# Kernel optimization log

Measured on AMD Instinct MI355X. Metric: run time of the kernel, lower is better.

## Reference

```python
import jax, jax.numpy as jnp
import numpy as np

NUM_NODES = 4
D = 1024            # hidden dim and dims of s_0, s_1; initial_input_dims = [D, D, 2D]
NUM_OPS = 5         # candidate ops per MixedLayer: linear, relu, tanh, sigmoid, leaky_relu(0.2)
NUM_LAYERS = 18     # sum_{i<4} (i+3)
BATCH = 4096

_ACTS = [
    lambda h: h,
    jax.nn.relu,
    jnp.tanh,
    jax.nn.sigmoid,
    lambda h: jax.nn.leaky_relu(h, 0.2),
]

def setup_inputs() -> dict:
    key = jax.random.key(0)
    ks = jax.random.split(key, 7)
    s_0 = jax.random.normal(ks[0], (BATCH, D), jnp.float32)
    s_1 = jax.random.normal(ks[1], (BATCH, D), jnp.float32)
    genotype = jax.random.uniform(ks[2], (NUM_LAYERS, NUM_OPS), jnp.float32)
    genotype = genotype / genotype.sum(-1, keepdims=True)  # softmax-like arch weights
    scale = 1.0 / np.sqrt(D)
    # 14 layers take a D-dim input; 4 layers (the cat(s_0,s_1) edge of each node) take 2D
    Ws = jax.random.normal(ks[3], (14, NUM_OPS, D, D), jnp.float32) * scale
    Wb = jax.random.normal(ks[4], (4, NUM_OPS, 2 * D, D), jnp.float32) * (scale / np.sqrt(2.0))
    bs = jax.random.normal(ks[5], (NUM_LAYERS, NUM_OPS, D), jnp.float32) * 0.01
    return {"s_0": s_0, "s_1": s_1, "genotype": genotype, "Ws": Ws, "Wb": Wb, "bs": bs}

def _mixed(x, W, b, w):
    # x: [B, in], W: [K, in, D], b: [K, D], w: [K]
    h = jnp.einsum('bi,kio->kbo', x, W) + b[:, None, :]
    out = 0.0
    for k, act in enumerate(_ACTS):
        out = out + w[k] * act(h[k])
    return out

def reference(s_0, s_1, genotype, Ws, Wb, bs):
    states = [s_0, s_1, jnp.concatenate([s_0, s_1], axis=-1)]
    offset, si, bi = 0, 0, 0
    for i in range(NUM_NODES):
        s = 0.0
        for j, cur in enumerate(states):
            l = offset + j
            if j == 2:  # edge from cat(s_0, s_1): input dim 2D
                W = Wb[bi]; bi += 1
            else:
                W = Ws[si]; si += 1
            s = s + _mixed(cur, W, bs[l], genotype[l])
        offset += len(states)
        states.append(s)
    return states[-1]
```

## Files before the change

### kernel.cpp

```cpp
#include <hip/hip_runtime.h>
#include <hip/hip_bf16.h>
#include <cstdint>
#include <cstddef>

typedef __attribute__((ext_vector_type(8))) short bf16x8;
typedef __attribute__((ext_vector_type(4))) float f32x4;

#define DEV __device__ __forceinline__

DEV unsigned short f2bf(float f) {
  unsigned int u = __float_as_uint(f);
  return (unsigned short)((u + 0x7fffu + ((u >> 16) & 1u)) >> 16);
}

DEV void gl_lds16(const unsigned short* g, unsigned short* l) {
  __builtin_amdgcn_global_load_lds(
      (__attribute__((address_space(1))) const void*)g,
      (__attribute__((address_space(3))) void*)l, 16, 0, 0);
}

__global__ __launch_bounds__(256) void cvt_kernel(const float* __restrict__ src,
                                                  unsigned short* __restrict__ dst) {
  size_t i = (size_t)blockIdx.x * 256 + threadIdx.x;
  float4 v = ((const float4*)src)[i];
  ushort4 o;
  o.x = f2bf(v.x); o.y = f2bf(v.y); o.z = f2bf(v.z); o.w = f2bf(v.w);
  ((ushort4*)dst)[i] = o;
}

__global__ __launch_bounds__(256) void zero_kernel(float* __restrict__ p) {
  size_t i = (size_t)blockIdx.x * 256 + threadIdx.x;
  ((float4*)p)[i] = make_float4(0.f, 0.f, 0.f, 0.f);
}

__global__ __launch_bounds__(256) void cvtzero_kernel(float* __restrict__ s,
                                                      unsigned short* __restrict__ dst) {
  size_t i = (size_t)blockIdx.x * 256 + threadIdx.x;
  float4 v = ((float4*)s)[i];
  ushort4 o;
  o.x = f2bf(v.x); o.y = f2bf(v.y); o.z = f2bf(v.z); o.w = f2bf(v.w);
  ((ushort4*)dst)[i] = o;
  ((float4*)s)[i] = make_float4(0.f, 0.f, 0.f, 0.f);
}

__global__ __launch_bounds__(256) void transpose_kernel(const float* __restrict__ src,
                                                        unsigned short* __restrict__ dst,
                                                        int K) {
  __shared__ float tile[64][68];
  const int t = threadIdx.x;
  const int tpm = (K >> 6) * 16;
  const int mat = blockIdx.x / tpm;
  const int r = blockIdx.x % tpm;
  const int tk = r >> 4;
  const int tn = r & 15;
  const size_t sbase = (size_t)mat * K * 1024 + (size_t)tk * 64 * 1024 + (size_t)tn * 64;
#pragma unroll
  for (int p = 0; p < 4; ++p) {
    int row = p * 16 + (t >> 4);
    int c4 = (t & 15) * 4;
    float4 v = *(const float4*)&src[sbase + (size_t)row * 1024 + c4];
    *(float4*)&tile[row][c4] = v;
  }
  __syncthreads();
  const int kbase = tk * 64;
  const size_t dbase = (size_t)mat * 1024 * K + (size_t)(kbase >> 10) * 1024 * 1024 +
                       (size_t)tn * 64 * 1024 + (size_t)(kbase & 1023);
#pragma unroll
  for (int p = 0; p < 4; ++p) {
    int n = p * 16 + (t >> 4);
    int k4 = (t & 15) * 4;
    ushort4 o;
    o.x = f2bf(tile[k4 + 0][n]);
    o.y = f2bf(tile[k4 + 1][n]);
    o.z = f2bf(tile[k4 + 2][n]);
    o.w = f2bf(tile[k4 + 3][n]);
    *(ushort4*)&dst[dbase + (size_t)n * 1024 + k4] = o;
  }
}

struct SegCfg {
  const unsigned short* x;
  const unsigned short* w;
  size_t wops;
  int l;
  int last;
};
struct NodeArgs {
  SegCfg s[7];
  int nseg;
};

__global__ __launch_bounds__(256, 2) void node_gemm(NodeArgs na,
                                                    const float* __restrict__ genotype,
                                                    const float* __restrict__ bs,
                                                    float* __restrict__ sout) {
  __shared__ unsigned short lds[16384];

  const int t = threadIdx.x;
  const int lane = t & 63;
  const int w = t >> 6;
  const int wm = (w & 1) * 64;
  const int wn = (w >> 1) * 64;
  const int bn = blockIdx.x * 128;
  const int bm = blockIdx.y * 128;
  const int kop = blockIdx.z;
  const int l15 = lane & 15;
  const int l16 = lane >> 4;

  const int srow = ((t >> 5) << 3) | (t & 7);
  const int schunk = (t >> 3) & 3;
  const size_t aoffg = (size_t)(bm + srow) * 1024 + schunk * 8;
  const size_t boffg = (size_t)(bn + srow) * 1024 + schunk * 8;

  unsigned short* dA0 = lds + t * 8;
  unsigned short* dB0 = lds + 4096 + t * 8;
  unsigned short* dA1 = lds + 8192 + t * 8;
  unsigned short* dB1 = lds + 12288 + t * 8;

  int aof[4], bof[4];
#pragma unroll
  for (int mi = 0; mi < 4; ++mi) {
    int r = wm + mi * 16 + l15;
    aof[mi] = (r >> 3) * 256 + l16 * 64 + (r & 7) * 8;
  }
#pragma unroll
  for (int ni = 0; ni < 4; ++ni) {
    int r = wn + ni * 16 + l15;
    bof[ni] = (r >> 3) * 256 + l16 * 64 + (r & 7) * 8;
  }

  f32x4 sacc[4][4];
  f32x4 hacc[4][4];
#pragma unroll
  for (int mi = 0; mi < 4; ++mi)
#pragma unroll
    for (int ni = 0; ni < 4; ++ni) {
      sacc[mi][ni] = (f32x4){0.f, 0.f, 0.f, 0.f};
      hacc[mi][ni] = (f32x4){0.f, 0.f, 0.f, 0.f};
    }

  auto stage = [&](const unsigned short* pa, const unsigned short* pb,
                   unsigned short* da, unsigned short* db) {
    gl_lds16(pa, da);
    gl_lds16(pa + 64 * 1024, da + 2048);
    gl_lds16(pb, db);
    gl_lds16(pb + 64 * 1024, db + 2048);
  };

  auto compute = [&](const unsigned short* Ab, const unsigned short* Bb) {
    bf16x8 af[4], bfr[4];
#pragma unroll
    for (int mi = 0; mi < 4; ++mi) af[mi] = *(const bf16x8*)&Ab[aof[mi]];
#pragma unroll
    for (int ni = 0; ni < 4; ++ni) bfr[ni] = *(const bf16x8*)&Bb[bof[ni]];
#pragma unroll
    for (int mi = 0; mi < 4; ++mi)
#pragma unroll
      for (int ni = 0; ni < 4; ++ni)
        hacc[mi][ni] = __builtin_amdgcn_mfma_f32_16x16x32_bf16(af[mi], bfr[ni],
                                                               hacc[mi][ni], 0, 0, 0);
  };

  auto epilogue = [&](int l) {
    const float wlk = genotype[l * 5 + kop];
    const float* bv = bs + ((size_t)l * 5 + kop) * 1024;
#pragma unroll
    for (int ni = 0; ni < 4; ++ni) {
      const float bias = bv[bn + wn + ni * 16 + l15];
#pragma unroll
      for (int mi = 0; mi < 4; ++mi)
#pragma unroll
        for (int i = 0; i < 4; ++i) {
          float h = hacc[mi][ni][i] + bias;
          float a;
          if (kop == 0) a = h;
          else if (kop == 1) a = fmaxf(h, 0.f);
          else if (kop == 2) a = 1.f - 2.f / (__expf(2.f * h) + 1.f);
          else if (kop == 3) a = 1.f / (1.f + __expf(-h));
          else a = (h > 0.f) ? h : 0.2f * h;
          sacc[mi][ni][i] += wlk * a;
          hacc[mi][ni][i] = 0.f;
        }
    }
  };

  const unsigned short* pa = na.s[0].x + aoffg;
  const unsigned short* pb = na.s[0].w + (size_t)kop * na.s[0].wops + boffg;
  int cl = na.s[0].l, clast = na.s[0].last;
  stage(pa, pb, dA0, dB0);
  __syncthreads();

  for (int e = 0; e < na.nseg; ++e) {
#pragma unroll 1
    for (int kt2 = 0; kt2 < 15; ++kt2) {
      stage(pa + (2 * kt2 + 1) * 32, pb + (2 * kt2 + 1) * 32, dA1, dB1);
      compute(lds, lds + 4096);
      __syncthreads();
      stage(pa + (2 * kt2 + 2) * 32, pb + (2 * kt2 + 2) * 32, dA0, dB0);
      compute(lds + 8192, lds + 12288);
      __syncthreads();
    }
    stage(pa + 31 * 32, pb + 31 * 32, dA1, dB1);
    compute(lds, lds + 4096);
    __syncthreads();
    if (e + 1 < na.nseg) {
      pa = na.s[e + 1].x + aoffg;
      pb = na.s[e + 1].w + (size_t)kop * na.s[e + 1].wops + boffg;
      stage(pa, pb, dA0, dB0);
    }
    compute(lds + 8192, lds + 12288);
    if (clast) epilogue(cl);
    if (e + 1 < na.nseg) {
      cl = na.s[e + 1].l;
      clast = na.s[e + 1].last;
    }
    __syncthreads();
  }

#pragma unroll
  for (int mi = 0; mi < 4; ++mi)
#pragma unroll
    for (int ni = 0; ni < 4; ++ni)
#pragma unroll
      for (int i = 0; i < 4; ++i) {
        const int row = bm + wm + mi * 16 + l16 * 4 + i;
        const int col = bn + wn + ni * 16 + l15;
        unsafeAtomicAdd(&sout[(size_t)row * 1024 + col], sacc[mi][ni][i]);
      }
}

extern "C" void kernel_launch(void* const* d_in, const int* in_sizes, int n_in,
                              void* d_out, int out_size, void* d_ws, size_t ws_size,
                              hipStream_t stream) {
  const float* s0 = (const float*)d_in[0];
  const float* s1 = (const float*)d_in[1];
  const float* geno = (const float*)d_in[2];
  const float* Ws = (const float*)d_in[3];
  const float* Wb = (const float*)d_in[4];
  const float* bs = (const float*)d_in[5];

  unsigned short* WsT = (unsigned short*)d_ws;
  unsigned short* WbT = WsT + 70ull * 1024 * 1024;
  unsigned short* S0 = WbT + 20ull * 2048 * 1024;
  unsigned short* S1 = S0 + 4096ull * 1024;
  unsigned short* T0 = S1 + 4096ull * 1024;
  unsigned short* T1 = T0 + 4096ull * 1024;
  unsigned short* T2 = T1 + 4096ull * 1024;
  float* S = (float*)(T2 + 4096ull * 1024);

  cvt_kernel<<<4096, 256, 0, stream>>>(s0, S0);
  cvt_kernel<<<4096, 256, 0, stream>>>(s1, S1);
  zero_kernel<<<4096, 256, 0, stream>>>(S);
  zero_kernel<<<4096, 256, 0, stream>>>((float*)d_out);
  transpose_kernel<<<70 * 256, 256, 0, stream>>>(Ws, WsT, 1024);
  transpose_kernel<<<20 * 512, 256, 0, stream>>>(Wb, WbT, 2048);

  auto SS = [&](const unsigned short* x, int si, int l) {
    SegCfg c;
    c.x = x;
    c.w = WsT + (size_t)si * 5 * 1024 * 1024;
    c.wops = (size_t)1024 * 1024;
    c.l = l; c.last = 1;
    return c;
  };
  auto BH = [&](int bi, int half, int l) {
    SegCfg c;
    c.x = half ? S1 : S0;
    c.w = WbT + (size_t)bi * 5 * 2048 * 1024 + (size_t)half * 1024 * 1024;
    c.wops = (size_t)2048 * 1024;
    c.l = l; c.last = half;
    return c;
  };

  dim3 grid(8, 32, 5);
  {
    NodeArgs a{}; a.nseg = 4;
    a.s[0] = SS(S0, 0, 0); a.s[1] = SS(S1, 1, 1);
    a.s[2] = BH(0, 0, 2); a.s[3] = BH(0, 1, 2);
    node_gemm<<<grid, 256, 0, stream>>>(a, geno, bs, S);
    cvtzero_kernel<<<4096, 256, 0, stream>>>(S, T0);
  }
  {
    NodeArgs a{}; a.nseg = 5;
    a.s[0] = SS(S0, 2, 3); a.s[1] = SS(S1, 3, 4);
    a.s[2] = BH(1, 0, 5); a.s[3] = BH(1, 1, 5);
    a.s[4] = SS(T0, 4, 6);
    node_gemm<<<grid, 256, 0, stream>>>(a, geno, bs, S);
    cvtzero_kernel<<<4096, 256, 0, stream>>>(S, T1);
  }
  {
    NodeArgs a{}; a.nseg = 6;
    a.s[0] = SS(S0, 5, 7); a.s[1] = SS(S1, 6, 8);
    a.s[2] = BH(2, 0, 9); a.s[3] = BH(2, 1, 9);
    a.s[4] = SS(T0, 7, 10); a.s[5] = SS(T1, 8, 11);
    node_gemm<<<grid, 256, 0, stream>>>(a, geno, bs, S);
    cvtzero_kernel<<<4096, 256, 0, stream>>>(S, T2);
  }
  {
    NodeArgs a{}; a.nseg = 7;
    a.s[0] = SS(S0, 9, 12); a.s[1] = SS(S1, 10, 13);
    a.s[2] = BH(3, 0, 14); a.s[3] = BH(3, 1, 14);
    a.s[4] = SS(T0, 11, 15); a.s[5] = SS(T1, 12, 16); a.s[6] = SS(T2, 13, 17);
    node_gemm<<<grid, 256, 0, stream>>>(a, geno, bs, (float*)d_out);
  }
}
```

Measured before the change: 2.826 ms.

## Deepen GEMM pipeline to four LDS stages with explicit waitcnt scheduling

Replaces the double-buffered LDS pipeline with a 4-stage ring buffer (64KB LDS). Each step waits with vmcnt(12), issues the next global-to-LDS loads right after the fragment reads, and continues prefetching across segment boundaries. Bias and genotype values are preloaded into registers, and the kernel is templated on the segment count. The intent is to hide global memory latency better, at the cost of doubled LDS use, which may cut occupancy from 2 blocks/CU, and more fragile hand-written barrier and waitcnt ordering. The last segment prefetches segment 0 again, which is wasted traffic.

```diff
diff --git a/kernel.cpp b/kernel.cpp
--- a/kernel.cpp
+++ b/kernel.cpp
@@ -90,11 +90,39 @@
   int nseg;
 };
 
+#define PIPE_STEP(BUF, SA, SB)                                                   \
+  {                                                                              \
+    asm volatile("s_waitcnt vmcnt(12)" ::: "memory");                            \
+    __builtin_amdgcn_s_barrier();                                                \
+    __builtin_amdgcn_sched_barrier(0);                                           \
+    bf16x8 af[4], bfr[4];                                                        \
+    _Pragma("unroll") for (int mi = 0; mi < 4; ++mi)                             \
+        af[mi] = *(const bf16x8*)&lds[(BUF) * 8192 + aof[mi]];                   \
+    _Pragma("unroll") for (int ni = 0; ni < 4; ++ni)                             \
+        bfr[ni] = *(const bf16x8*)&lds[(BUF) * 8192 + 4096 + bof[ni]];           \
+    asm volatile("s_waitcnt lgkmcnt(0)" ::: "memory");                           \
+    __builtin_amdgcn_sched_barrier(0);                                           \
+    __builtin_amdgcn_s_barrier();                                                \
+    __builtin_amdgcn_sched_barrier(0);                                           \
+    {                                                                            \
+      unsigned short* da = lds + (BUF) * 8192 + t * 8;                           \
+      gl_lds16((SA), da);                                                        \
+      gl_lds16((SA) + 64 * 1024, da + 2048);                                     \
+      gl_lds16((SB), da + 4096);                                                 \
+      gl_lds16((SB) + 64 * 1024, da + 6144);                                     \
+    }                                                                            \
+    _Pragma("unroll") for (int mi = 0; mi < 4; ++mi)                             \
+        _Pragma("unroll") for (int ni = 0; ni < 4; ++ni)                         \
+            hacc[mi][ni] = __builtin_amdgcn_mfma_f32_16x16x32_bf16(              \
+                af[mi], bfr[ni], hacc[mi][ni], 0, 0, 0);                         \
+  }
+
+template <int NSEG>
 __global__ __launch_bounds__(256, 2) void node_gemm(NodeArgs na,
                                                     const float* __restrict__ genotype,
                                                     const float* __restrict__ bs,
                                                     float* __restrict__ sout) {
-  __shared__ unsigned short lds[16384];
+  __shared__ unsigned short lds[32768];
 
   const int t = threadIdx.x;
   const int lane = t & 63;
@@ -112,11 +140,6 @@
   const size_t aoffg = (size_t)(bm + srow) * 1024 + schunk * 8;
   const size_t boffg = (size_t)(bn + srow) * 1024 + schunk * 8;
 
-  unsigned short* dA0 = lds + t * 8;
-  unsigned short* dB0 = lds + 4096 + t * 8;
-  unsigned short* dA1 = lds + 8192 + t * 8;
-  unsigned short* dB1 = lds + 12288 + t * 8;
-
   int aof[4], bof[4];
 #pragma unroll
   for (int mi = 0; mi < 4; ++mi) {
@@ -127,6 +150,17 @@
   for (int ni = 0; ni < 4; ++ni) {
     int r = wn + ni * 16 + l15;
     bof[ni] = (r >> 3) * 256 + l16 * 64 + (r & 7) * 8;
+  }
+
+  float br[NSEG][4];
+  float wl[NSEG];
+#pragma unroll
+  for (int e = 0; e < NSEG; ++e) {
+    const int l = na.s[e].l;
+    wl[e] = genotype[l * 5 + kop];
+#pragma unroll
+    for (int ni = 0; ni < 4; ++ni)
+      br[e][ni] = bs[((size_t)l * 5 + kop) * 1024 + bn + wn + ni * 16 + l15];
   }
 
   f32x4 sacc[4][4];
@@ -139,82 +173,58 @@
       hacc[mi][ni] = (f32x4){0.f, 0.f, 0.f, 0.f};
     }
 
-  auto stage = [&](const unsigned short* pa, const unsigned short* pb,
-                   unsigned short* da, unsigned short* db) {
-    gl_lds16(pa, da);
-    gl_lds16(pa + 64 * 1024, da + 2048);
-    gl_lds16(pb, db);
-    gl_lds16(pb + 64 * 1024, db + 2048);
-  };
-
-  auto compute = [&](const unsigned short* Ab, const unsigned short* Bb) {
-    bf16x8 af[4], bfr[4];
-#pragma unroll
-    for (int mi = 0; mi < 4; ++mi) af[mi] = *(const bf16x8*)&Ab[aof[mi]];
-#pragma unroll
-    for (int ni = 0; ni < 4; ++ni) bfr[ni] = *(const bf16x8*)&Bb[bof[ni]];
-#pragma unroll
-    for (int mi = 0; mi < 4; ++mi)
-#pragma unroll
-      for (int ni = 0; ni < 4; ++ni)
-        hacc[mi][ni] = __builtin_amdgcn_mfma_f32_16x16x32_bf16(af[mi], bfr[ni],
-                                                               hacc[mi][ni], 0, 0, 0);
-  };
-
-  auto epilogue = [&](int l) {
-    const float wlk = genotype[l * 5 + kop];
-    const float* bv = bs + ((size_t)l * 5 + kop) * 1024;
-#pragma unroll
-    for (int ni = 0; ni < 4; ++ni) {
-      const float bias = bv[bn + wn + ni * 16 + l15];
-#pragma unroll
-      for (int mi = 0; mi < 4; ++mi)
-#pragma unroll
-        for (int i = 0; i < 4; ++i) {
-          float h = hacc[mi][ni][i] + bias;
-          float a;
-          if (kop == 0) a = h;
-          else if (kop == 1) a = fmaxf(h, 0.f);
-          else if (kop == 2) a = 1.f - 2.f / (__expf(2.f * h) + 1.f);
-          else if (kop == 3) a = 1.f / (1.f + __expf(-h));
-          else a = (h > 0.f) ? h : 0.2f * h;
-          sacc[mi][ni][i] += wlk * a;
-          hacc[mi][ni][i] = 0.f;
-        }
+  {
+    const unsigned short* pa0 = na.s[0].x + aoffg;
+    const unsigned short* pb0 = na.s[0].w + (size_t)kop * na.s[0].wops + boffg;
+#pragma unroll
+    for (int i = 0; i < 4; ++i) {
+      unsigned short* da = lds + i * 8192 + t * 8;
+      gl_lds16(pa0 + i * 32, da);
+      gl_lds16(pa0 + i * 32 + 64 * 1024, da + 2048);
+      gl_lds16(pb0 + i * 32, da + 4096);
+      gl_lds16(pb0 + i * 32 + 64 * 1024, da + 6144);
     }
-  };
-
-  const unsigned short* pa = na.s[0].x + aoffg;
-  const unsigned short* pb = na.s[0].w + (size_t)kop * na.s[0].wops + boffg;
-  int cl = na.s[0].l, clast = na.s[0].last;
-  stage(pa, pb, dA0, dB0);
-  __syncthreads();
-
-  for (int e = 0; e < na.nseg; ++e) {
+  }
+
+#pragma unroll
+  for (int e = 0; e < NSEG; ++e) {
+    const unsigned short* pa = na.s[e].x + aoffg;
+    const unsigned short* pb = na.s[e].w + (size_t)kop * na.s[e].wops + boffg;
+    const int en = (e + 1 < NSEG) ? e + 1 : 0;
+    const unsigned short* pna = na.s[en].x + aoffg;
+    const unsigned short* pnb = na.s[en].w + (size_t)kop * na.s[en].wops + boffg;
+
 #pragma unroll 1
-    for (int kt2 = 0; kt2 < 15; ++kt2) {
-      stage(pa + (2 * kt2 + 1) * 32, pb + (2 * kt2 + 1) * 32, dA1, dB1);
-      compute(lds, lds + 4096);
-      __syncthreads();
-      stage(pa + (2 * kt2 + 2) * 32, pb + (2 * kt2 + 2) * 32, dA0, dB0);
-      compute(lds + 8192, lds + 12288);
-      __syncthreads();
+    for (int m = 0; m < 8; ++m) {
+      const unsigned short* spa = (m < 7) ? (pa + (size_t)(4 * m + 4) * 32) : pna;
+      const unsigned short* spb = (m < 7) ? (pb + (size_t)(4 * m + 4) * 32) : pnb;
+      PIPE_STEP(0, spa, spb)
+      PIPE_STEP(1, spa + 32, spb + 32)
+      PIPE_STEP(2, spa + 64, spb + 64)
+      PIPE_STEP(3, spa + 96, spb + 96)
     }
-    stage(pa + 31 * 32, pb + 31 * 32, dA1, dB1);
-    compute(lds, lds + 4096);
-    __syncthreads();
-    if (e + 1 < na.nseg) {
-      pa = na.s[e + 1].x + aoffg;
-      pb = na.s[e + 1].w + (size_t)kop * na.s[e + 1].wops + boffg;
-      stage(pa, pb, dA0, dB0);
+
+    if (na.s[e].last) {
+      const float wlk = wl[e];
+#pragma unroll
+      for (int ni = 0; ni < 4; ++ni) {
+        const float bias = br[e][ni];
+#pragma unroll
+        for (int mi = 0; mi < 4; ++mi)
+#pragma unroll
+          for (int i = 0; i < 4; ++i) {
+            float h = hacc[mi][ni][i] + bias;
+            float a;
+            if (kop == 0) a = h;
+            else if (kop == 1) a = fmaxf(h, 0.f);
+            else if (kop == 2) a = 1.f - 2.f / (__expf(2.f * h) + 1.f);
+            else if (kop == 3) a = 1.f / (1.f + __expf(-h));
+            else a = (h > 0.f) ? h : 0.2f * h;
+            sacc[mi][ni][i] += wlk * a;
+            hacc[mi][ni][i] = 0.f;
+          }
+      }
     }
-    compute(lds + 8192, lds + 12288);
-    if (clast) epilogue(cl);
-    if (e + 1 < na.nseg) {
-      cl = na.s[e + 1].l;
-      clast = na.s[e + 1].last;
-    }
-    __syncthreads();
   }
 
 #pragma unroll
@@ -277,7 +287,7 @@
     NodeArgs a{}; a.nseg = 4;
     a.s[0] = SS(S0, 0, 0); a.s[1] = SS(S1, 1, 1);
     a.s[2] = BH(0, 0, 2); a.s[3] = BH(0, 1, 2);
-    node_gemm<<<grid, 256, 0, stream>>>(a, geno, bs, S);
+    node_gemm<4><<<grid, 256, 0, stream>>>(a, geno, bs, S);
     cvtzero_kernel<<<4096, 256, 0, stream>>>(S, T0);
   }
   {
@@ -285,7 +295,7 @@
     a.s[0] = SS(S0, 2, 3); a.s[1] = SS(S1, 3, 4);
     a.s[2] = BH(1, 0, 5); a.s[3] = BH(1, 1, 5);
     a.s[4] = SS(T0, 4, 6);
-    node_gemm<<<grid, 256, 0, stream>>>(a, geno, bs, S);
+    node_gemm<5><<<grid, 256, 0, stream>>>(a, geno, bs, S);
     cvtzero_kernel<<<4096, 256, 0, stream>>>(S, T1);
   }
   {
@@ -293,7 +303,7 @@
     a.s[0] = SS(S0, 5, 7); a.s[1] = SS(S1, 6, 8);
     a.s[2] = BH(2, 0, 9); a.s[3] = BH(2, 1, 9);
     a.s[4] = SS(T0, 7, 10); a.s[5] = SS(T1, 8, 11);
-    node_gemm<<<grid, 256, 0, stream>>>(a, geno, bs, S);
+    node_gemm<6><<<grid, 256, 0, stream>>>(a, geno, bs, S);
     cvtzero_kernel<<<4096, 256, 0, stream>>>(S, T2);
   }
   {
@@ -301,6 +311,6 @@
     a.s[0] = SS(S0, 9, 12); a.s[1] = SS(S1, 10, 13);
     a.s[2] = BH(3, 0, 14); a.s[3] = BH(3, 1, 14);
     a.s[4] = SS(T0, 11, 15); a.s[5] = SS(T1, 12, 16); a.s[6] = SS(T2, 13, 17);
-    node_gemm<<<grid, 256, 0, stream>>>(a, geno, bs, (float*)d_out);
-  }
-}
+    node_gemm<7><<<grid, 256, 0, stream>>>(a, geno, bs, (float*)d_out);
+  }
+}
```

After: 2.483 ms. -12.1%, faster.
